# Optimization experiments

Measured on AMD Instinct MI355X. Metric: run time of the kernel, lower is better.

Reference implementation:

```python
import jax, jax.numpy as jnp
import numpy as np

# Circuit structure constants (must match input_specs)
V, K, C = 128, 32, 256   # vars, input nodes per var, categories (V*K == N)
L, N, F = 4, 4096, 16    # layer pairs, sum nodes per layer, sum fan-in
E, B = 8192, 512         # product elements per layer, batch size
EPS = 1e-6


def setup_inputs() -> dict:
    key = jax.random.key(0)
    ks = jax.random.split(key, 6)
    return {
        "inputs": jax.random.randint(ks[0], (B, V), 0, C),
        "prod_child_ids": jax.random.randint(ks[1], (L, E, 2), 0, N),
        "sum_child_ids": jax.random.randint(ks[2], (L, N, F), 0, E),
        "input_params": jax.random.uniform(ks[3], (V, K, C), dtype=jnp.float32),
        "sum_params": jax.random.uniform(ks[4], (L, N, F), dtype=jnp.float32),
        "root_params": jax.random.uniform(ks[5], (N,), dtype=jnp.float32),
    }


def _forward(inputs, prod_child_ids, sum_child_ids, input_params, sum_params, root_params):
    # --- input layer: categorical leaves -> node_mars [V*K, B] (log space) ---
    lw_in = jnp.log(input_params + EPS)
    lw_in = lw_in - jax.nn.logsumexp(lw_in, axis=-1, keepdims=True)  # normalized log-params
    x = inputs.T  # [V, B]
    nm = lw_in[jnp.arange(V)[:, None, None], jnp.arange(K)[None, :, None], x[:, None, :]]  # [V, K, B]
    nm = nm.reshape(V * K, B)  # node_mars for leaves, V*K == N

    # --- normalized sum-layer log-weights ---
    lw_sum = jnp.log(sum_params + EPS)
    lw_sum = lw_sum - jax.nn.logsumexp(lw_sum, axis=-1, keepdims=True)  # [L, N, F]

    # --- alternating prod / sum layer groups (fixed small L) ---
    for l in range(L):
        # product layer: element_mars[e] = sum of child node_mars (log space add)
        em = nm[prod_child_ids[l, :, 0]] + nm[prod_child_ids[l, :, 1]]  # [E, B]
        # sum layer: node_mars[n] = logsumexp_j(element_mars[child j] + log w[n, j])
        ch = em[sum_child_ids[l]]  # [N, F, B] irregular gather
        nm = jax.nn.logsumexp(ch + lw_sum[l][:, :, None], axis=1)  # [N, B]

    # --- root sum node -> log-likelihoods [B] ---
    lr = jnp.log(root_params + EPS)
    lr = lr - jax.nn.logsumexp(lr)
    return jax.nn.logsumexp(nm + lr[:, None], axis=0)  # [B]


def reference(inputs, prod_child_ids, sum_child_ids, input_params, sum_params, root_params):
    return _forward(inputs, prod_child_ids, sum_child_ids, input_params, sum_params, root_params)
```

## Files before the change

### kernel.cpp

```cpp
#include <hip/hip_runtime.h>
#include <hip/hip_fp16.h>
#include <math.h>

#define V_ 128
#define K_ 32
#define C_ 256
#define L_ 4
#define N_ 4096
#define F_ 16
#define E_ 8192
#define B_ 512
#define EPS_ 1e-6f

__device__ __forceinline__ __half2 u2h(unsigned u) {
    __half2 h; *reinterpret_cast<unsigned*>(&h) = u; return h;
}
__device__ __forceinline__ unsigned h2u(__half2 h) {
    return *reinterpret_cast<unsigned*>(&h);
}
__device__ __forceinline__ __half b2h(unsigned short u) {
    __half h; *reinterpret_cast<unsigned short*>(&h) = u; return h;
}
__device__ __forceinline__ unsigned short h2b(__half h) {
    return *reinterpret_cast<unsigned short*>(&h);
}
__device__ __forceinline__ __half2 hmax2(__half2 a, __half2 b) {
    float2 fa = __half22float2(a), fb = __half22float2(b);
    return __floats2half2_rn(fmaxf(fa.x, fb.x), fmaxf(fa.y, fb.y));
}

__global__ __launch_bounds__(256) void prep_kernel(const float* __restrict__ sp,
                                                   const int* __restrict__ prod,
                                                   const int* __restrict__ sc,
                                                   const float* __restrict__ ip,
                                                   const float* __restrict__ rp,
                                                   unsigned* __restrict__ PIW,
                                                   unsigned* __restrict__ PP,
                                                   float* __restrict__ inv_row,
                                                   float* __restrict__ lrpsum) {
    int blk = blockIdx.x;
    int tid = threadIdx.x;
    if (blk < 64) {
        int idx = blk * 256 + tid;
        int l   = idx >> 12;
        int n   = idx & (N_ - 1);
        const float4* row4 = (const float4*)(sp + (size_t)idx * F_);
        float v[F_];
        float s = 0.f;
#pragma unroll
        for (int q = 0; q < 4; q++) {
            float4 r = row4[q];
            v[4*q+0] = r.x + EPS_; v[4*q+1] = r.y + EPS_;
            v[4*q+2] = r.z + EPS_; v[4*q+3] = r.w + EPS_;
            s += v[4*q+0] + v[4*q+1] + v[4*q+2] + v[4*q+3];
        }
        float inv = 1.f / s;
        const int* scr = sc + (size_t)idx * F_;
#pragma unroll
        for (int f = 0; f < F_; f++) {
            unsigned wbits = h2b(__float2half(v[f] * inv));
            PIW[((size_t)l * F_ + f) * N_ + n] =
                (unsigned)(unsigned short)scr[f] | (wbits << 16);
        }
    } else if (blk < 192) {
        int idx = (blk - 64) * 256 + tid;
        int2 c  = ((const int2*)prod)[idx];
        PP[idx] = (unsigned)c.x | ((unsigned)c.y << 16);
    } else if (blk < 192 + 1024) {
        int rblk = blk - 192;
        int n    = rblk * 4 + (tid >> 6);
        int lane = tid & 63;
        const float* row = ip + (size_t)n * C_;
        float t = 0.f;
#pragma unroll
        for (int i = 0; i < 4; i++) t += row[lane + 64 * i] + EPS_;
#pragma unroll
        for (int off = 32; off; off >>= 1) t += __shfl_down(t, off, 64);
        if (lane == 0) inv_row[n] = 1.f / t;
    } else {
        __shared__ float smem[4];
        float acc = 0.f;
        for (int i = tid; i < N_; i += 256) acc += rp[i] + EPS_;
#pragma unroll
        for (int off = 32; off; off >>= 1) acc += __shfl_down(acc, off, 64);
        if ((tid & 63) == 0) smem[tid >> 6] = acc;
        __syncthreads();
        if (tid == 0) lrpsum[0] = __logf(smem[0] + smem[1] + smem[2] + smem[3]);
    }
}

__global__ __launch_bounds__(1024) void mega_kernel(const float* __restrict__ ip,
                                                    const int* __restrict__ inputs,
                                                    const float* __restrict__ inv_row,
                                                    const float* __restrict__ rp,
                                                    const unsigned* __restrict__ PIW,
                                                    const unsigned* __restrict__ PP,
                                                    const float* __restrict__ lrpsum,
                                                    float* __restrict__ out) {
    __shared__ unsigned nm[N_];
    __shared__ unsigned em[E_];
    __shared__ unsigned redm[16];
    __shared__ float    redf[32];
    int tid  = threadIdx.x;
    int lane = tid & 63;
    int w    = tid >> 6;
    int b0   = blockIdx.x * 2, b1 = b0 + 1;

    float2 u[4];
    float mx0 = 0.f, mx1 = 0.f;
#pragma unroll
    for (int p = 0; p < 4; p++) {
        int n  = p * 1024 + tid;
        int v  = n >> 5;
        int x0 = inputs[b0 * V_ + v];
        int x1 = inputs[b1 * V_ + v];
        float invr = inv_row[n];
        u[p].x = (ip[(size_t)n * C_ + x0] + EPS_) * invr;
        u[p].y = (ip[(size_t)n * C_ + x1] + EPS_) * invr;
        mx0 = fmaxf(mx0, u[p].x);
        mx1 = fmaxf(mx1, u[p].y);
    }
#pragma unroll
    for (int off = 32; off; off >>= 1) {
        mx0 = fmaxf(mx0, __shfl_down(mx0, off, 64));
        mx1 = fmaxf(mx1, __shfl_down(mx1, off, 64));
    }
    if (lane == 0) { redf[w] = mx0; redf[16 + w] = mx1; }
    __syncthreads();
    float m0 = redf[0], m1 = redf[16];
#pragma unroll
    for (int i = 1; i < 16; i++) { m0 = fmaxf(m0, redf[i]); m1 = fmaxf(m1, redf[16 + i]); }
    float inv0 = 1.f / m0, inv1 = 1.f / m1;
    float sg0 = -__logf(inv0), sg1 = -__logf(inv1);
#pragma unroll
    for (int p = 0; p < 4; p++)
        nm[p * 1024 + tid] = h2u(__floats2half2_rn(u[p].x * inv0, u[p].y * inv1));
    __syncthreads();

    for (int l = 0; l < L_ - 1; l++) {
        const unsigned* pp = PP + (size_t)l * E_;
#pragma unroll
        for (int p = 0; p < 8; p++) {
            int e = p * 1024 + tid;
            unsigned c = pp[e];
            em[e] = h2u(__hmul2(u2h(nm[c & 0xffff]), u2h(nm[c >> 16])));
        }
        __syncthreads();

        const unsigned* piw = PIW + (size_t)l * F_ * N_;
        unsigned o[4];
        __half2  hm = u2h(0u);
#pragma unroll
        for (int p = 0; p < 4; p++) {
            int n = p * 1024 + tid;
            unsigned q[F_];
#pragma unroll
            for (int f = 0; f < F_; f++) q[f] = piw[f * N_ + n];
            __half2 acc = u2h(0u);
#pragma unroll
            for (int f = 0; f < F_; f++)
                acc = __hfma2(u2h(em[q[f] & 0xffff]),
                              __half2half2(b2h((unsigned short)(q[f] >> 16))), acc);
            o[p] = h2u(acc);
            hm   = hmax2(hm, acc);
        }
#pragma unroll
        for (int off = 32; off; off >>= 1)
            hm = hmax2(hm, u2h(__shfl_down(h2u(hm), off, 64)));
        if (lane == 0) redm[w] = h2u(hm);
        __syncthreads();
        __half2 M = u2h(redm[0]);
#pragma unroll
        for (int i = 1; i < 16; i++) M = hmax2(M, u2h(redm[i]));
        float M0 = __half2float(__low2half(M)), M1 = __half2float(__high2half(M));
        __half2 hi = __floats2half2_rn(1.f / M0, 1.f / M1);
        float ai0 = __half2float(__low2half(hi)), ai1 = __half2float(__high2half(hi));
        sg0 = 2.f * sg0 - __logf(ai0);
        sg1 = 2.f * sg1 - __logf(ai1);
#pragma unroll
        for (int p = 0; p < 4; p++)
            nm[p * 1024 + tid] = h2u(__hmul2(u2h(o[p]), hi));
        __syncthreads();
    }

    {
        const unsigned* pp = PP + (size_t)(L_ - 1) * E_;
#pragma unroll
        for (int p = 0; p < 8; p++) {
            int e = p * 1024 + tid;
            unsigned c = pp[e];
            em[e] = h2u(__hmul2(u2h(nm[c & 0xffff]), u2h(nm[c >> 16])));
        }
        __syncthreads();

        const unsigned* piw = PIW + (size_t)(L_ - 1) * F_ * N_;
        float S0 = 0.f, S1 = 0.f;
#pragma unroll
        for (int p = 0; p < 4; p++) {
            int n = p * 1024 + tid;
            unsigned q[F_];
#pragma unroll
            for (int f = 0; f < F_; f++) q[f] = piw[f * N_ + n];
            __half2 acc = u2h(0u);
#pragma unroll
            for (int f = 0; f < F_; f++)
                acc = __hfma2(u2h(em[q[f] & 0xffff]),
                              __half2half2(b2h((unsigned short)(q[f] >> 16))), acc);
            float2 vv = __half22float2(acc);
            float  r  = rp[n] + EPS_;
            S0 += r * vv.x;
            S1 += r * vv.y;
        }
        float sgf0 = 2.f * sg0, sgf1 = 2.f * sg1;
#pragma unroll
        for (int off = 32; off; off >>= 1) {
            S0 += __shfl_down(S0, off, 64);
            S1 += __shfl_down(S1, off, 64);
        }
        if (lane == 0) { redf[w] = S0; redf[16 + w] = S1; }
        __syncthreads();
        if (tid == 0) {
            float s0 = 0.f, s1 = 0.f;
#pragma unroll
            for (int i = 0; i < 16; i++) { s0 += redf[i]; s1 += redf[16 + i]; }
            float lr = lrpsum[0];
            out[b0] = __logf(s0) + sgf0 - lr;
            out[b1] = __logf(s1) + sgf1 - lr;
        }
    }
}

extern "C" void kernel_launch(void* const* d_in, const int* in_sizes, int n_in,
                              void* d_out, int out_size, void* d_ws, size_t ws_size,
                              hipStream_t stream) {
    const int*   inputs = (const int*)d_in[0];
    const int*   prod   = (const int*)d_in[1];
    const int*   sc     = (const int*)d_in[2];
    const float* ip     = (const float*)d_in[3];
    const float* sp     = (const float*)d_in[4];
    const float* rp     = (const float*)d_in[5];
    float* out = (float*)d_out;

    unsigned* PIW     = (unsigned*)d_ws;
    unsigned* PP      = PIW + (size_t)L_ * F_ * N_;
    float*    inv_row = (float*)(PP + (size_t)L_ * E_);
    float*    lrpsum  = inv_row + N_;

    prep_kernel<<<64 + 128 + 1024 + 1, 256, 0, stream>>>(sp, prod, sc, ip, rp,
                                                         PIW, PP, inv_row, lrpsum);
    mega_kernel<<<B_ / 2, 1024, 0, stream>>>(ip, inputs, inv_row, rp,
                                             PIW, PP, lrpsum, out);
}
```

Before: 108.0 us.

## Store sum-edge table node-major and fold per-layer rescale into product gather

The packed sum-edge table (child index plus fp16 weight) is now stored per node, so each thread loads its 16 edges as four uint4 vector loads instead of 16 strided scalar loads. Product-layer child index pairs are also read four at a time as uint4. The per-layer max normalization no longer rewrites node_mars in a separate pass. The scale factor is applied lazily while gathering children in the next product layer, which removes one barrier and one LDS read/write pass per layer. In exchange, the log-scale bookkeeping becomes harder to follow, there are extra half multiplies, and unnormalized fp16 values are stored between layers, with the scale clamped to avoid overflow.

```diff
diff --git a/kernel.cpp b/kernel.cpp
--- a/kernel.cpp
+++ b/kernel.cpp
@@ -42,8 +42,6 @@
     int tid = threadIdx.x;
     if (blk < 64) {
         int idx = blk * 256 + tid;
-        int l   = idx >> 12;
-        int n   = idx & (N_ - 1);
         const float4* row4 = (const float4*)(sp + (size_t)idx * F_);
         float v[F_];
         float s = 0.f;
@@ -56,11 +54,11 @@
         }
         float inv = 1.f / s;
         const int* scr = sc + (size_t)idx * F_;
+        unsigned* dst  = PIW + (size_t)idx * F_;
 #pragma unroll
         for (int f = 0; f < F_; f++) {
             unsigned wbits = h2b(__float2half(v[f] * inv));
-            PIW[((size_t)l * F_ + f) * N_ + n] =
-                (unsigned)(unsigned short)scr[f] | (wbits << 16);
+            dst[f] = (unsigned)(unsigned short)scr[f] | (wbits << 16);
         }
     } else if (blk < 192) {
         int idx = (blk - 64) * 256 + tid;
@@ -131,38 +129,62 @@
 #pragma unroll
     for (int i = 1; i < 16; i++) { m0 = fmaxf(m0, redf[i]); m1 = fmaxf(m1, redf[16 + i]); }
     float inv0 = 1.f / m0, inv1 = 1.f / m1;
-    float sg0 = -__logf(inv0), sg1 = -__logf(inv1);
+    float sg0 = __logf(m0), sg1 = __logf(m1);
 #pragma unroll
     for (int p = 0; p < 4; p++)
         nm[p * 1024 + tid] = h2u(__floats2half2_rn(u[p].x * inv0, u[p].y * inv1));
     __syncthreads();
 
+    __half2 ha  = __floats2half2_rn(1.f, 1.f);
+    float   af0 = 1.f, af1 = 1.f;
+
     for (int l = 0; l < L_ - 1; l++) {
-        const unsigned* pp = PP + (size_t)l * E_;
-#pragma unroll
-        for (int p = 0; p < 8; p++) {
-            int e = p * 1024 + tid;
-            unsigned c = pp[e];
-            em[e] = h2u(__hmul2(u2h(nm[c & 0xffff]), u2h(nm[c >> 16])));
-        }
-        __syncthreads();
-
-        const unsigned* piw = PIW + (size_t)l * F_ * N_;
-        unsigned o[4];
-        __half2  hm = u2h(0u);
+        const uint4* pp4 = (const uint4*)(PP + (size_t)l * E_);
+#pragma unroll
+        for (int p = 0; p < 2; p++) {
+            uint4 c = pp4[p * 1024 + tid];
+            int e   = (p * 1024 + tid) * 4;
+            em[e+0] = h2u(__hmul2(__hmul2(u2h(nm[c.x & 0xffff]), ha),
+                                  __hmul2(u2h(nm[c.x >> 16]), ha)));
+            em[e+1] = h2u(__hmul2(__hmul2(u2h(nm[c.y & 0xffff]), ha),
+                                  __hmul2(u2h(nm[c.y >> 16]), ha)));
+            em[e+2] = h2u(__hmul2(__hmul2(u2h(nm[c.z & 0xffff]), ha),
+                                  __hmul2(u2h(nm[c.z >> 16]), ha)));
+            em[e+3] = h2u(__hmul2(__hmul2(u2h(nm[c.w & 0xffff]), ha),
+                                  __hmul2(u2h(nm[c.w >> 16]), ha)));
+        }
+        sg0 = 2.f * sg0 + 2.f * __logf(af0);
+        sg1 = 2.f * sg1 + 2.f * __logf(af1);
+        sg0 -= 4.f * __logf(af0) * 0.f;
+        __syncthreads();
+
+        const unsigned* piw = PIW + (size_t)l * N_ * F_;
+        __half2 hm = u2h(0u);
 #pragma unroll
         for (int p = 0; p < 4; p++) {
             int n = p * 1024 + tid;
-            unsigned q[F_];
-#pragma unroll
-            for (int f = 0; f < F_; f++) q[f] = piw[f * N_ + n];
+            const uint4* qv = (const uint4*)(piw + (size_t)n * F_);
+            uint4 q0 = qv[0], q1 = qv[1], q2 = qv[2], q3 = qv[3];
             __half2 acc = u2h(0u);
-#pragma unroll
-            for (int f = 0; f < F_; f++)
-                acc = __hfma2(u2h(em[q[f] & 0xffff]),
-                              __half2half2(b2h((unsigned short)(q[f] >> 16))), acc);
-            o[p] = h2u(acc);
-            hm   = hmax2(hm, acc);
+            unsigned qq;
+            qq = q0.x; acc = __hfma2(u2h(em[qq & 0xffff]), __half2half2(b2h((unsigned short)(qq >> 16))), acc);
+            qq = q0.y; acc = __hfma2(u2h(em[qq & 0xffff]), __half2half2(b2h((unsigned short)(qq >> 16))), acc);
+            qq = q0.z; acc = __hfma2(u2h(em[qq & 0xffff]), __half2half2(b2h((unsigned short)(qq >> 16))), acc);
+            qq = q0.w; acc = __hfma2(u2h(em[qq & 0xffff]), __half2half2(b2h((unsigned short)(qq >> 16))), acc);
+            qq = q1.x; acc = __hfma2(u2h(em[qq & 0xffff]), __half2half2(b2h((unsigned short)(qq >> 16))), acc);
+            qq = q1.y; acc = __hfma2(u2h(em[qq & 0xffff]), __half2half2(b2h((unsigned short)(qq >> 16))), acc);
+            qq = q1.z; acc = __hfma2(u2h(em[qq & 0xffff]), __half2half2(b2h((unsigned short)(qq >> 16))), acc);
+            qq = q1.w; acc = __hfma2(u2h(em[qq & 0xffff]), __half2half2(b2h((unsigned short)(qq >> 16))), acc);
+            qq = q2.x; acc = __hfma2(u2h(em[qq & 0xffff]), __half2half2(b2h((unsigned short)(qq >> 16))), acc);
+            qq = q2.y; acc = __hfma2(u2h(em[qq & 0xffff]), __half2half2(b2h((unsigned short)(qq >> 16))), acc);
+            qq = q2.z; acc = __hfma2(u2h(em[qq & 0xffff]), __half2half2(b2h((unsigned short)(qq >> 16))), acc);
+            qq = q2.w; acc = __hfma2(u2h(em[qq & 0xffff]), __half2half2(b2h((unsigned short)(qq >> 16))), acc);
+            qq = q3.x; acc = __hfma2(u2h(em[qq & 0xffff]), __half2half2(b2h((unsigned short)(qq >> 16))), acc);
+            qq = q3.y; acc = __hfma2(u2h(em[qq & 0xffff]), __half2half2(b2h((unsigned short)(qq >> 16))), acc);
+            qq = q3.z; acc = __hfma2(u2h(em[qq & 0xffff]), __half2half2(b2h((unsigned short)(qq >> 16))), acc);
+            qq = q3.w; acc = __hfma2(u2h(em[qq & 0xffff]), __half2half2(b2h((unsigned short)(qq >> 16))), acc);
+            nm[n] = h2u(acc);
+            hm    = hmax2(hm, acc);
         }
 #pragma unroll
         for (int off = 32; off; off >>= 1)
@@ -173,45 +195,62 @@
 #pragma unroll
         for (int i = 1; i < 16; i++) M = hmax2(M, u2h(redm[i]));
         float M0 = __half2float(__low2half(M)), M1 = __half2float(__high2half(M));
-        __half2 hi = __floats2half2_rn(1.f / M0, 1.f / M1);
-        float ai0 = __half2float(__low2half(hi)), ai1 = __half2float(__high2half(hi));
-        sg0 = 2.f * sg0 - __logf(ai0);
-        sg1 = 2.f * sg1 - __logf(ai1);
-#pragma unroll
-        for (int p = 0; p < 4; p++)
-            nm[p * 1024 + tid] = h2u(__hmul2(u2h(o[p]), hi));
-        __syncthreads();
+        ha  = __floats2half2_rn(fminf(1.f / M0, 60000.f), fminf(1.f / M1, 60000.f));
+        af0 = __half2float(__low2half(ha));
+        af1 = __half2float(__high2half(ha));
+        sg0 -= 2.f * __logf(af0);
+        sg1 -= 2.f * __logf(af1);
     }
 
     {
-        const unsigned* pp = PP + (size_t)(L_ - 1) * E_;
-#pragma unroll
-        for (int p = 0; p < 8; p++) {
-            int e = p * 1024 + tid;
-            unsigned c = pp[e];
-            em[e] = h2u(__hmul2(u2h(nm[c & 0xffff]), u2h(nm[c >> 16])));
-        }
-        __syncthreads();
-
-        const unsigned* piw = PIW + (size_t)(L_ - 1) * F_ * N_;
+        const uint4* pp4 = (const uint4*)(PP + (size_t)(L_ - 1) * E_);
+#pragma unroll
+        for (int p = 0; p < 2; p++) {
+            uint4 c = pp4[p * 1024 + tid];
+            int e   = (p * 1024 + tid) * 4;
+            em[e+0] = h2u(__hmul2(__hmul2(u2h(nm[c.x & 0xffff]), ha),
+                                  __hmul2(u2h(nm[c.x >> 16]), ha)));
+            em[e+1] = h2u(__hmul2(__hmul2(u2h(nm[c.y & 0xffff]), ha),
+                                  __hmul2(u2h(nm[c.y >> 16]), ha)));
+            em[e+2] = h2u(__hmul2(__hmul2(u2h(nm[c.z & 0xffff]), ha),
+                                  __hmul2(u2h(nm[c.z >> 16]), ha)));
+            em[e+3] = h2u(__hmul2(__hmul2(u2h(nm[c.w & 0xffff]), ha),
+                                  __hmul2(u2h(nm[c.w >> 16]), ha)));
+        }
+        sg0 = 2.f * sg0 + 2.f * __logf(af0);
+        sg1 = 2.f * sg1 + 2.f * __logf(af1);
+        __syncthreads();
+
+        const unsigned* piw = PIW + (size_t)(L_ - 1) * N_ * F_;
         float S0 = 0.f, S1 = 0.f;
 #pragma unroll
         for (int p = 0; p < 4; p++) {
             int n = p * 1024 + tid;
-            unsigned q[F_];
-#pragma unroll
-            for (int f = 0; f < F_; f++) q[f] = piw[f * N_ + n];
+            const uint4* qv = (const uint4*)(piw + (size_t)n * F_);
+            uint4 qa = qv[0], qb = qv[1], qc = qv[2], qd = qv[3];
             __half2 acc = u2h(0u);
-#pragma unroll
-            for (int f = 0; f < F_; f++)
-                acc = __hfma2(u2h(em[q[f] & 0xffff]),
-                              __half2half2(b2h((unsigned short)(q[f] >> 16))), acc);
+            unsigned qq;
+            qq = qa.x; acc = __hfma2(u2h(em[qq & 0xffff]), __half2half2(b2h((unsigned short)(qq >> 16))), acc);
+            qq = qa.y; acc = __hfma2(u2h(em[qq & 0xffff]), __half2half2(b2h((unsigned short)(qq >> 16))), acc);
+            qq = qa.z; acc = __hfma2(u2h(em[qq & 0xffff]), __half2half2(b2h((unsigned short)(qq >> 16))), acc);
+            qq = qa.w; acc = __hfma2(u2h(em[qq & 0xffff]), __half2half2(b2h((unsigned short)(qq >> 16))), acc);
+            qq = qb.x; acc = __hfma2(u2h(em[qq & 0xffff]), __half2half2(b2h((unsigned short)(qq >> 16))), acc);
+            qq = qb.y; acc = __hfma2(u2h(em[qq & 0xffff]), __half2half2(b2h((unsigned short)(qq >> 16))), acc);
+            qq = qb.z; acc = __hfma2(u2h(em[qq & 0xffff]), __half2half2(b2h((unsigned short)(qq >> 16))), acc);
+            qq = qb.w; acc = __hfma2(u2h(em[qq & 0xffff]), __half2half2(b2h((unsigned short)(qq >> 16))), acc);
+            qq = qc.x; acc = __hfma2(u2h(em[qq & 0xffff]), __half2half2(b2h((unsigned short)(qq >> 16))), acc);
+            qq = qc.y; acc = __hfma2(u2h(em[qq & 0xffff]), __half2half2(b2h((unsigned short)(qq >> 16))), acc);
+            qq = qc.z; acc = __hfma2(u2h(em[qq & 0xffff]), __half2half2(b2h((unsigned short)(qq >> 16))), acc);
+            qq = qc.w; acc = __hfma2(u2h(em[qq & 0xffff]), __half2half2(b2h((unsigned short)(qq >> 16))), acc);
+            qq = qd.x; acc = __hfma2(u2h(em[qq & 0xffff]), __half2half2(b2h((unsigned short)(qq >> 16))), acc);
+            qq = qd.y; acc = __hfma2(u2h(em[qq & 0xffff]), __half2half2(b2h((unsigned short)(qq >> 16))), acc);
+            qq = qd.z; acc = __hfma2(u2h(em[qq & 0xffff]), __half2half2(b2h((unsigned short)(qq >> 16))), acc);
+            qq = qd.w; acc = __hfma2(u2h(em[qq & 0xffff]), __half2half2(b2h((unsigned short)(qq >> 16))), acc);
             float2 vv = __half22float2(acc);
             float  r  = rp[n] + EPS_;
             S0 += r * vv.x;
             S1 += r * vv.y;
         }
-        float sgf0 = 2.f * sg0, sgf1 = 2.f * sg1;
 #pragma unroll
         for (int off = 32; off; off >>= 1) {
             S0 += __shfl_down(S0, off, 64);
@@ -224,8 +263,8 @@
 #pragma unroll
             for (int i = 0; i < 16; i++) { s0 += redf[i]; s1 += redf[16 + i]; }
             float lr = lrpsum[0];
-            out[b0] = __logf(s0) + sgf0 - lr;
-            out[b1] = __logf(s1) + sgf1 - lr;
+            out[b0] = __logf(s0) + sg0 - lr;
+            out[b1] = __logf(s1) + sg1 - lr;
         }
     }
 }
@@ -242,7 +281,7 @@
     float* out = (float*)d_out;
 
     unsigned* PIW     = (unsigned*)d_ws;
-    unsigned* PP      = PIW + (size_t)L_ * F_ * N_;
+    unsigned* PP      = PIW + (size_t)L_ * N_ * F_;
     float*    inv_row = (float*)(PP + (size_t)L_ * E_);
     float*    lrpsum  = inv_row + N_;
 
```

Measured after the change: 106.9 us. No clear change (-1.0%).
